# Kernel optimization log

Measured on AMD Instinct MI355X. Metric: run time of the kernel, lower is better.

Reference implementation:

```python
import jax, jax.numpy as jnp
import numpy as np

ALPHA = 0.25
GAMMA = 2.0
B, A, C, M = 8, 120000, 80, 32


def setup_inputs() -> dict:
    key = jax.random.key(0)
    k1, k2, k3, k4, k5, k6 = jax.random.split(key, 6)
    classifications = jax.random.uniform(k1, (B, A, C), jnp.float32)
    regressions = jax.random.normal(k2, (B, A, 4), jnp.float32)
    # anchors: valid x1<x2, y1<y2 boxes in a 1024x1024 image
    cx = jax.random.uniform(k3, (A,), jnp.float32, 0.0, 1024.0)
    cy = jax.random.uniform(k4, (A,), jnp.float32, 0.0, 1024.0)
    w = jax.random.uniform(jax.random.fold_in(k3, 1), (A,), jnp.float32, 16.0, 256.0)
    h = jax.random.uniform(jax.random.fold_in(k4, 1), (A,), jnp.float32, 16.0, 256.0)
    anchors = jnp.stack([cx - 0.5 * w, cy - 0.5 * h, cx + 0.5 * w, cy + 0.5 * h], axis=1)[None]
    # annotations: [x1,y1,x2,y2,label], all valid (label in [0, C))
    gcx = jax.random.uniform(k5, (B, M), jnp.float32, 64.0, 960.0)
    gcy = jax.random.uniform(jax.random.fold_in(k5, 1), (B, M), jnp.float32, 64.0, 960.0)
    gw = jax.random.uniform(jax.random.fold_in(k5, 2), (B, M), jnp.float32, 16.0, 256.0)
    gh = jax.random.uniform(jax.random.fold_in(k5, 3), (B, M), jnp.float32, 16.0, 256.0)
    labels = jax.random.randint(k6, (B, M), 0, C).astype(jnp.float32)
    annotations = jnp.stack(
        [gcx - 0.5 * gw, gcy - 0.5 * gh, gcx + 0.5 * gw, gcy + 0.5 * gh, labels], axis=2)
    return dict(classifications=classifications, regressions=regressions,
                anchors=anchors, annotations=annotations)


def _calc_iou(a, b):
    # a: [A,4] anchors, b: [M,4] gt boxes -> [A,M]
    area = (b[:, 2] - b[:, 0]) * (b[:, 3] - b[:, 1])
    iw = jnp.minimum(a[:, 2, None], b[None, :, 2]) - jnp.maximum(a[:, 0, None], b[None, :, 0])
    ih = jnp.minimum(a[:, 3, None], b[None, :, 3]) - jnp.maximum(a[:, 1, None], b[None, :, 1])
    inter = jnp.clip(iw, 0.0) * jnp.clip(ih, 0.0)
    ua = ((a[:, 2] - a[:, 0]) * (a[:, 3] - a[:, 1]))[:, None] + area[None, :] - inter
    return inter / jnp.clip(ua, 1e-8)


def _per_image(cls, reg, annots, anchor):
    valid = annots[:, 4] != -1.0  # padded gt boxes (label == -1) are ignored
    num_valid = valid.sum()
    cls = jnp.clip(cls, 1e-4, 1.0 - 1e-4)
    iou = jnp.where(valid[None, :], _calc_iou(anchor, annots[:, :4]), -1.0)  # [A,M]
    iou_max = iou.max(axis=1)
    iou_argmax = iou.argmax(axis=1)
    positive = iou_max >= 0.5
    num_pos = positive.sum()
    assigned = annots[iou_argmax]  # [A,5]
    nclass = cls.shape[1]
    # targets: -1 ignore; 0 where IoU<0.4 or positive; one-hot 1 at gt class for positives
    targets = jnp.full(cls.shape, -1.0, cls.dtype)
    targets = jnp.where((iou_max < 0.4)[:, None], 0.0, targets)
    onehot = jax.nn.one_hot(assigned[:, 4].astype(jnp.int32), nclass, dtype=cls.dtype)
    targets = jnp.where(positive[:, None], onehot, targets)
    alpha_factor = jnp.where(targets == 1.0, ALPHA, 1.0 - ALPHA)
    focal_w = alpha_factor * jnp.where(targets == 1.0, 1.0 - cls, cls) ** GAMMA
    bce = -(targets * jnp.log(cls) + (1.0 - targets) * jnp.log(1.0 - cls))
    cls_loss_mat = jnp.where(targets != -1.0, focal_w * bce, 0.0)
    npos_f = num_pos.astype(cls.dtype)
    cls_loss = cls_loss_mat.sum() / jnp.maximum(npos_f, 1.0)
    aw = anchor[:, 2] - anchor[:, 0]
    ah = anchor[:, 3] - anchor[:, 1]
    acx = anchor[:, 0] + 0.5 * aw
    acy = anchor[:, 1] + 0.5 * ah
    gw = assigned[:, 2] - assigned[:, 0]
    gh = assigned[:, 3] - assigned[:, 1]
    gcx = assigned[:, 0] + 0.5 * gw
    gcy = assigned[:, 1] + 0.5 * gh
    gw = jnp.maximum(gw, 1.0)
    gh = jnp.maximum(gh, 1.0)
    t = jnp.stack([(gcx - acx) / aw, (gcy - acy) / ah,
                   jnp.log(gw / aw), jnp.log(gh / ah)], axis=1)
    t = t / jnp.array([[0.1, 0.1, 0.2, 0.2]], t.dtype)
    diff = jnp.abs(t - reg)
    rl = jnp.where(diff <= 1.0 / 9.0, 0.5 * 9.0 * diff * diff, diff - 0.5 / 9.0)
    rl = jnp.where(positive[:, None], rl, 0.0)
    reg_loss = rl.sum() / jnp.maximum(npos_f * 4.0, 1.0)  # mean over [num_pos,4]
    reg_loss = jnp.where(num_pos > 0, reg_loss, 0.0)
    has = num_valid > 0
    return jnp.where(has, cls_loss, 0.0), jnp.where(has, reg_loss, 0.0)


def reference(classifications, regressions, anchors, annotations):
    anchor = anchors[0]
    cls_l, reg_l = jax.vmap(lambda c, r, a: _per_image(c, r, a, anchor))(
        classifications, regressions, annotations)
    return cls_l.mean(keepdims=True), reg_l.mean(keepdims=True)
```

## Files before the change

kernel.cpp:

```cpp
#include <hip/hip_runtime.h>

constexpr int B_IMG = 8;
constexpr int A_N   = 120000;
constexpr int C_N   = 80;
constexpr int M_N   = 32;

constexpr float ALPHA = 0.25f;

constexpr int BLK  = 256;
constexpr int APB  = 256;
constexpr int NBLK = (A_N + APB - 1) / APB;
constexpr int F4PA = C_N / 4;
constexpr int U    = 5;
constexpr int F4_PER_IT = BLK * U;
constexpr int NIT  = (APB * F4PA) / F4_PER_IT;

typedef float f4v __attribute__((ext_vector_type(4)));

__device__ __forceinline__ float smooth_l1(float d) {
    d = fabsf(d);
    return (d <= (1.0f / 9.0f)) ? 4.5f * d * d : d - (0.5f / 9.0f);
}

__device__ __forceinline__ float loss_neg(float x) {
    float p = fminf(fmaxf(x, 1e-4f), 0.9999f);
    return (1.0f - ALPHA) * p * p * (-__logf(1.0f - p));
}

__device__ __forceinline__ float loss_neg4(f4v v) {
    return loss_neg(v[0]) + loss_neg(v[1]) + loss_neg(v[2]) + loss_neg(v[3]);
}

__device__ __forceinline__ float loss_pos(float x) {
    float p = fminf(fmaxf(x, 1e-4f), 0.9999f);
    float q = 1.0f - p;
    return ALPHA * q * q * (-__logf(p));
}

__global__ __launch_bounds__(BLK, 4) void fused_kernel(
    const float* __restrict__ cls,
    const float* __restrict__ regressions,
    const float* __restrict__ anchors,
    const float* __restrict__ annotations,
    float* __restrict__ clsPart,
    float* __restrict__ regPart,
    float* __restrict__ nposPart)
{
    const int b    = blockIdx.y;
    const int base = blockIdx.x * APB;
    const int nA   = min(APB, A_N - base);
    const int t    = threadIdx.x;
    const int wave = t >> 6;
    const int lane = t & 63;
    const int a    = base + t;
    const bool full = (nA == APB);
    const bool inA  = (t < nA);

    __shared__ float smask[APB];

    const float* __restrict__ rowbase = cls + (size_t)(b * A_N + base) * C_N;
    const f4v* __restrict__ src = (const f4v*)rowbase;
    const f4v* __restrict__ pw = src + wave * (64 * U) + lane;
    const int widx0 = wave * (64 * U) + lane;

    float4 anc = make_float4(0.f, 0.f, 0.f, 0.f);
    if (inA) anc = ((const float4*)anchors)[a];

    f4v vA[U], vB[U];
    if (full) {
        #pragma unroll
        for (int u = 0; u < U; ++u) vA[u] = pw[u * 64];
        #pragma unroll
        for (int u = 0; u < U; ++u) vB[u] = pw[F4_PER_IT + u * 64];
    }

    const float* __restrict__ ann = annotations + (size_t)b * M_N * 5;
    int  bm = -1;
    bool positive = false, ignored = false;
    if (inA) {
        const float ax1 = anc.x, ay1 = anc.y, ax2 = anc.z, ay2 = anc.w;
        const float areaA = (ax2 - ax1) * (ay2 - ay1);
        float bi = -1.0f, bu = 1.0f;
        #pragma unroll 2
        for (int m = 0; m < M_N; ++m) {
            const float gx1 = ann[m * 5 + 0];
            const float gy1 = ann[m * 5 + 1];
            const float gx2 = ann[m * 5 + 2];
            const float gy2 = ann[m * 5 + 3];
            const bool valid = (ann[m * 5 + 4] != -1.0f);
            float iw = fminf(ax2, gx2) - fmaxf(ax1, gx1);
            float ih = fminf(ay2, gy2) - fmaxf(ay1, gy1);
            iw = fmaxf(iw, 0.0f);
            ih = fmaxf(ih, 0.0f);
            const float inter = iw * ih;
            const float areaB = (gx2 - gx1) * (gy2 - gy1);
            const float ua = fmaxf(areaA + areaB - inter, 1e-8f);
            const bool better = valid && (inter * bu > bi * ua);
            if (better) { bi = inter; bu = ua; bm = m; }
        }
        const float iouMax = (bm >= 0) ? (bi / bu) : -1.0f;
        positive = (iouMax >= 0.5f);
        ignored  = (iouMax >= 0.4f) && !positive;
    }
    smask[t] = (inA && !ignored) ? 1.0f : 0.0f;

    float regl = 0.0f, csum = 0.0f;
    const float pos = positive ? 1.0f : 0.0f;
    if (positive) {
        const float ax1 = anc.x, ay1 = anc.y, ax2 = anc.z, ay2 = anc.w;
        const float aw  = ax2 - ax1;
        const float ah  = ay2 - ay1;
        const float acx = ax1 + 0.5f * aw;
        const float acy = ay1 + 0.5f * ah;
        const float gx1 = ann[bm * 5 + 0];
        const float gy1 = ann[bm * 5 + 1];
        const float gx2 = ann[bm * 5 + 2];
        const float gy2 = ann[bm * 5 + 3];
        float gw = gx2 - gx1;
        float gh = gy2 - gy1;
        const float gcx = gx1 + 0.5f * gw;
        const float gcy = gy1 + 0.5f * gh;
        gw = fmaxf(gw, 1.0f);
        gh = fmaxf(gh, 1.0f);
        const float t0 = ((gcx - acx) / aw) * 10.0f;
        const float t1 = ((gcy - acy) / ah) * 10.0f;
        const float t2 = __logf(gw / aw) * 5.0f;
        const float t3 = __logf(gh / ah) * 5.0f;
        const float4 rg = ((const float4*)regressions)[(size_t)b * A_N + a];
        regl = smooth_l1(t0 - rg.x) + smooth_l1(t1 - rg.y) +
               smooth_l1(t2 - rg.z) + smooth_l1(t3 - rg.w);

        const int code = (int)ann[bm * 5 + 4];
        const float x = rowbase[(size_t)t * C_N + code];
        csum += loss_pos(x) - loss_neg(x);
    }
    __syncthreads();

    if (full) {
        #pragma unroll 1
        for (int it2 = 0; it2 < NIT / 2; ++it2) {
            const int it = it2 * 2;
            float pa = 0.0f;
            #pragma unroll
            for (int u = 0; u < U; ++u) {
                const unsigned idx = (unsigned)(it * F4_PER_IT + widx0 + u * 64);
                pa += smask[idx / 20u] * loss_neg4(vA[u]);
            }
            if (it + 2 < NIT) {
                #pragma unroll
                for (int u = 0; u < U; ++u)
                    vA[u] = pw[(it + 2) * F4_PER_IT + u * 64];
            }
            csum += pa;
            float pb = 0.0f;
            #pragma unroll
            for (int u = 0; u < U; ++u) {
                const unsigned idx = (unsigned)((it + 1) * F4_PER_IT + widx0 + u * 64);
                pb += smask[idx / 20u] * loss_neg4(vB[u]);
            }
            if (it + 3 < NIT) {
                #pragma unroll
                for (int u = 0; u < U; ++u)
                    vB[u] = pw[(it + 3) * F4_PER_IT + u * 64];
            }
            csum += pb;
        }
    } else {
        const int nF4 = nA * F4PA;
        for (int idx = t; idx < nF4; idx += BLK)
            csum += smask[(unsigned)idx / 20u] * loss_neg4(src[idx]);
    }

    float r = regl, p = pos, c = csum;
    #pragma unroll
    for (int off = 32; off; off >>= 1) {
        r += __shfl_down(r, off);
        p += __shfl_down(p, off);
        c += __shfl_down(c, off);
    }
    __shared__ float wr[BLK / 64], wp[BLK / 64], wc[BLK / 64];
    if (lane == 0) { wr[wave] = r; wp[wave] = p; wc[wave] = c; }
    __syncthreads();
    if (t == 0) {
        float rr = 0.0f, pp = 0.0f, cc = 0.0f;
        #pragma unroll
        for (int w = 0; w < BLK / 64; ++w) { rr += wr[w]; pp += wp[w]; cc += wc[w]; }
        const int pidx = b * NBLK + blockIdx.x;
        clsPart[pidx]  = cc;
        regPart[pidx]  = rr;
        nposPart[pidx] = pp;
    }
}

__global__ __launch_bounds__(64 * B_IMG) void finalize_kernel(
    const float* __restrict__ annotations,
    const float* __restrict__ clsPart,
    const float* __restrict__ regPart,
    const float* __restrict__ nposPart,
    float* __restrict__ out)
{
    const int w    = threadIdx.x >> 6;
    const int lane = threadIdx.x & 63;

    float c = 0.0f, r = 0.0f, p = 0.0f;
    for (int i = lane; i < NBLK; i += 64) {
        const int idx = w * NBLK + i;
        c += clsPart[idx];
        r += regPart[idx];
        p += nposPart[idx];
    }
    #pragma unroll
    for (int off = 32; off; off >>= 1) {
        c += __shfl_down(c, off);
        r += __shfl_down(r, off);
        p += __shfl_down(p, off);
    }

    __shared__ float sc[B_IMG], sr[B_IMG];
    if (lane == 0) {
        bool has = false;
        for (int m = 0; m < M_N; ++m)
            has = has || (annotations[(size_t)w * M_N * 5 + m * 5 + 4] != -1.0f);
        const float cl = c / fmaxf(p, 1.0f);
        const float rl = (p > 0.0f) ? r / (p * 4.0f) : 0.0f;
        sc[w] = has ? cl : 0.0f;
        sr[w] = has ? rl : 0.0f;
    }
    __syncthreads();
    if (threadIdx.x == 0) {
        float ca = 0.0f, ra = 0.0f;
        #pragma unroll
        for (int i = 0; i < B_IMG; ++i) { ca += sc[i]; ra += sr[i]; }
        out[0] = ca * (1.0f / B_IMG);
        out[1] = ra * (1.0f / B_IMG);
    }
}

extern "C" void kernel_launch(void* const* d_in, const int* in_sizes, int n_in,
                              void* d_out, int out_size, void* d_ws, size_t ws_size,
                              hipStream_t stream) {
    const float* classifications = (const float*)d_in[0];
    const float* regressions     = (const float*)d_in[1];
    const float* anchors         = (const float*)d_in[2];
    const float* annotations     = (const float*)d_in[3];
    float* out = (float*)d_out;

    float* clsPart  = (float*)d_ws;
    float* regPart  = clsPart + (size_t)B_IMG * NBLK;
    float* nposPart = regPart + (size_t)B_IMG * NBLK;

    fused_kernel<<<dim3(NBLK, B_IMG), BLK, 0, stream>>>(
        classifications, regressions, anchors, annotations,
        clsPart, regPart, nposPart);

    finalize_kernel<<<1, 64 * B_IMG, 0, stream>>>(
        annotations, clsPart, regPart, nposPart, out);
}
```

Measured before the change: 79.62 us.

## Fuse finalize into main kernel via last-block atomic, double anchors per block

The separate finalize kernel is removed: each workgroup writes its partials, fences, and bumps a global counter, and the last workgroup performs the final reduction. Each block now covers 512 anchors (two per thread for the IoU step) with a smaller unroll factor, which halves the grid and the number of partials. This targets the second kernel launch and its gap, but adds a memset before each call and an atomic per block. The larger per-block work also lowers the number of workgroups available for latency hiding.

```diff
diff --git a/kernel.cpp b/kernel.cpp
--- a/kernel.cpp
+++ b/kernel.cpp
@@ -8,10 +8,11 @@
 constexpr float ALPHA = 0.25f;
 
 constexpr int BLK  = 256;
-constexpr int APB  = 256;
+constexpr int APB  = 512;
 constexpr int NBLK = (A_N + APB - 1) / APB;
+constexpr int NWG  = NBLK * B_IMG;
 constexpr int F4PA = C_N / 4;
-constexpr int U    = 5;
+constexpr int U    = 4;
 constexpr int F4_PER_IT = BLK * U;
 constexpr int NIT  = (APB * F4PA) / F4_PER_IT;
 
@@ -35,6 +36,37 @@
     float p = fminf(fmaxf(x, 1e-4f), 0.9999f);
     float q = 1.0f - p;
     return ALPHA * q * q * (-__logf(p));
+}
+
+__device__ __forceinline__ void iou_one(
+    const float4 anc, const float* __restrict__ ann,
+    int& bm, bool& positive, bool& ignored)
+{
+    const float ax1 = anc.x, ay1 = anc.y, ax2 = anc.z, ay2 = anc.w;
+    const float areaA = (ax2 - ax1) * (ay2 - ay1);
+
+    float bi = -1.0f, bu = 1.0f;
+    bm = -1;
+    #pragma unroll 2
+    for (int m = 0; m < M_N; ++m) {
+        const float gx1 = ann[m * 5 + 0];
+        const float gy1 = ann[m * 5 + 1];
+        const float gx2 = ann[m * 5 + 2];
+        const float gy2 = ann[m * 5 + 3];
+        const bool valid = (ann[m * 5 + 4] != -1.0f);
+        float iw = fminf(ax2, gx2) - fmaxf(ax1, gx1);
+        float ih = fminf(ay2, gy2) - fmaxf(ay1, gy1);
+        iw = fmaxf(iw, 0.0f);
+        ih = fmaxf(ih, 0.0f);
+        const float inter = iw * ih;
+        const float areaB = (gx2 - gx1) * (gy2 - gy1);
+        const float ua = fmaxf(areaA + areaB - inter, 1e-8f);
+        const bool better = valid && (inter * bu > bi * ua);
+        if (better) { bi = inter; bu = ua; bm = m; }
+    }
+    const float iouMax = (bm >= 0) ? (bi / bu) : -1.0f;
+    positive = (iouMax >= 0.5f);
+    ignored  = (iouMax >= 0.4f) && !positive;
 }
 
 __global__ __launch_bounds__(BLK, 4) void fused_kernel(
@@ -42,29 +74,34 @@
     const float* __restrict__ regressions,
     const float* __restrict__ anchors,
     const float* __restrict__ annotations,
+    int*   __restrict__ counter,
     float* __restrict__ clsPart,
     float* __restrict__ regPart,
-    float* __restrict__ nposPart)
+    float* __restrict__ nposPart,
+    float* __restrict__ out)
 {
     const int b    = blockIdx.y;
     const int base = blockIdx.x * APB;
     const int nA   = min(APB, A_N - base);
+    const float* __restrict__ ann = annotations + (size_t)b * M_N * 5;
+
+    __shared__ float smask[APB];
+
     const int t    = threadIdx.x;
     const int wave = t >> 6;
     const int lane = t & 63;
-    const int a    = base + t;
     const bool full = (nA == APB);
-    const bool inA  = (t < nA);
-
-    __shared__ float smask[APB];
 
     const float* __restrict__ rowbase = cls + (size_t)(b * A_N + base) * C_N;
     const f4v* __restrict__ src = (const f4v*)rowbase;
     const f4v* __restrict__ pw = src + wave * (64 * U) + lane;
     const int widx0 = wave * (64 * U) + lane;
 
-    float4 anc = make_float4(0.f, 0.f, 0.f, 0.f);
-    if (inA) anc = ((const float4*)anchors)[a];
+    const bool v0 = (t < nA), v1 = (BLK + t < nA);
+    float4 anc0 = make_float4(0.f, 0.f, 0.f, 0.f);
+    float4 anc1 = anc0;
+    if (v0) anc0 = ((const float4*)anchors)[base + t];
+    if (v1) anc1 = ((const float4*)anchors)[base + BLK + t];
 
     f4v vA[U], vB[U];
     if (full) {
@@ -74,39 +111,24 @@
         for (int u = 0; u < U; ++u) vB[u] = pw[F4_PER_IT + u * 64];
     }
 
-    const float* __restrict__ ann = annotations + (size_t)b * M_N * 5;
-    int  bm = -1;
-    bool positive = false, ignored = false;
-    if (inA) {
-        const float ax1 = anc.x, ay1 = anc.y, ax2 = anc.z, ay2 = anc.w;
-        const float areaA = (ax2 - ax1) * (ay2 - ay1);
-        float bi = -1.0f, bu = 1.0f;
-        #pragma unroll 2
-        for (int m = 0; m < M_N; ++m) {
-            const float gx1 = ann[m * 5 + 0];
-            const float gy1 = ann[m * 5 + 1];
-            const float gx2 = ann[m * 5 + 2];
-            const float gy2 = ann[m * 5 + 3];
-            const bool valid = (ann[m * 5 + 4] != -1.0f);
-            float iw = fminf(ax2, gx2) - fmaxf(ax1, gx1);
-            float ih = fminf(ay2, gy2) - fmaxf(ay1, gy1);
-            iw = fmaxf(iw, 0.0f);
-            ih = fmaxf(ih, 0.0f);
-            const float inter = iw * ih;
-            const float areaB = (gx2 - gx1) * (gy2 - gy1);
-            const float ua = fmaxf(areaA + areaB - inter, 1e-8f);
-            const bool better = valid && (inter * bu > bi * ua);
-            if (better) { bi = inter; bu = ua; bm = m; }
-        }
-        const float iouMax = (bm >= 0) ? (bi / bu) : -1.0f;
-        positive = (iouMax >= 0.5f);
-        ignored  = (iouMax >= 0.4f) && !positive;
-    }
-    smask[t] = (inA && !ignored) ? 1.0f : 0.0f;
+    int  bm0, bm1;
+    bool pos0 = false, pos1 = false, ign0 = false, ign1 = false;
+    if (v0) iou_one(anc0, ann, bm0, pos0, ign0);
+    if (v1) iou_one(anc1, ann, bm1, pos1, ign1);
+    smask[t]       = (v0 && !ign0) ? 1.0f : 0.0f;
+    smask[BLK + t] = (v1 && !ign1) ? 1.0f : 0.0f;
+    __syncthreads();
 
     float regl = 0.0f, csum = 0.0f;
-    const float pos = positive ? 1.0f : 0.0f;
-    if (positive) {
+    float pcntf = (pos0 ? 1.0f : 0.0f) + (pos1 ? 1.0f : 0.0f);
+    #pragma unroll
+    for (int k = 0; k < 2; ++k) {
+        const bool  pos = k ? pos1 : pos0;
+        if (!pos) continue;
+        const int   bm  = k ? bm1  : bm0;
+        const float4 anc = k ? anc1 : anc0;
+        const int   li  = k * BLK + t;
+        const int   a   = base + li;
         const float ax1 = anc.x, ay1 = anc.y, ax2 = anc.z, ay2 = anc.w;
         const float aw  = ax2 - ax1;
         const float ah  = ay2 - ay1;
@@ -127,14 +149,13 @@
         const float t2 = __logf(gw / aw) * 5.0f;
         const float t3 = __logf(gh / ah) * 5.0f;
         const float4 rg = ((const float4*)regressions)[(size_t)b * A_N + a];
-        regl = smooth_l1(t0 - rg.x) + smooth_l1(t1 - rg.y) +
-               smooth_l1(t2 - rg.z) + smooth_l1(t3 - rg.w);
+        regl += smooth_l1(t0 - rg.x) + smooth_l1(t1 - rg.y) +
+                smooth_l1(t2 - rg.z) + smooth_l1(t3 - rg.w);
 
         const int code = (int)ann[bm * 5 + 4];
-        const float x = rowbase[(size_t)t * C_N + code];
+        const float x = rowbase[(size_t)li * C_N + code];
         csum += loss_pos(x) - loss_neg(x);
     }
-    __syncthreads();
 
     if (full) {
         #pragma unroll 1
@@ -167,11 +188,13 @@
         }
     } else {
         const int nF4 = nA * F4PA;
-        for (int idx = t; idx < nF4; idx += BLK)
-            csum += smask[(unsigned)idx / 20u] * loss_neg4(src[idx]);
-    }
-
-    float r = regl, p = pos, c = csum;
+        for (int idx = t; idx < nF4; idx += BLK) {
+            const f4v v = src[idx];
+            csum += smask[(unsigned)idx / 20u] * loss_neg4(v);
+        }
+    }
+
+    float r = regl, p = pcntf, c = csum;
     #pragma unroll
     for (int off = 32; off; off >>= 1) {
         r += __shfl_down(r, off);
@@ -181,6 +204,7 @@
     __shared__ float wr[BLK / 64], wp[BLK / 64], wc[BLK / 64];
     if (lane == 0) { wr[wave] = r; wp[wave] = p; wc[wave] = c; }
     __syncthreads();
+    __shared__ int isLast;
     if (t == 0) {
         float rr = 0.0f, pp = 0.0f, cc = 0.0f;
         #pragma unroll
@@ -189,50 +213,47 @@
         clsPart[pidx]  = cc;
         regPart[pidx]  = rr;
         nposPart[pidx] = pp;
-    }
-}
-
-__global__ __launch_bounds__(64 * B_IMG) void finalize_kernel(
-    const float* __restrict__ annotations,
-    const float* __restrict__ clsPart,
-    const float* __restrict__ regPart,
-    const float* __restrict__ nposPart,
-    float* __restrict__ out)
-{
-    const int w    = threadIdx.x >> 6;
-    const int lane = threadIdx.x & 63;
-
-    float c = 0.0f, r = 0.0f, p = 0.0f;
-    for (int i = lane; i < NBLK; i += 64) {
-        const int idx = w * NBLK + i;
-        c += clsPart[idx];
-        r += regPart[idx];
-        p += nposPart[idx];
-    }
-    #pragma unroll
-    for (int off = 32; off; off >>= 1) {
-        c += __shfl_down(c, off);
-        r += __shfl_down(r, off);
-        p += __shfl_down(p, off);
-    }
-
-    __shared__ float sc[B_IMG], sr[B_IMG];
-    if (lane == 0) {
-        bool has = false;
-        for (int m = 0; m < M_N; ++m)
-            has = has || (annotations[(size_t)w * M_N * 5 + m * 5 + 4] != -1.0f);
-        const float cl = c / fmaxf(p, 1.0f);
-        const float rl = (p > 0.0f) ? r / (p * 4.0f) : 0.0f;
-        sc[w] = has ? cl : 0.0f;
-        sr[w] = has ? rl : 0.0f;
+        __threadfence();
+        const int old = atomicAdd(counter, 1);
+        isLast = (old == NWG - 1) ? 1 : 0;
     }
     __syncthreads();
-    if (threadIdx.x == 0) {
-        float ca = 0.0f, ra = 0.0f;
-        #pragma unroll
-        for (int i = 0; i < B_IMG; ++i) { ca += sc[i]; ra += sr[i]; }
-        out[0] = ca * (1.0f / B_IMG);
-        out[1] = ra * (1.0f / B_IMG);
+
+    if (isLast) {
+        __threadfence();
+        __shared__ float sc[B_IMG], sr[B_IMG];
+        for (int w = wave; w < B_IMG; w += BLK / 64) {
+            float fc = 0.0f, fr = 0.0f, fp = 0.0f;
+            for (int i = lane; i < NBLK; i += 64) {
+                const int idx = w * NBLK + i;
+                fc += clsPart[idx];
+                fr += regPart[idx];
+                fp += nposPart[idx];
+            }
+            #pragma unroll
+            for (int off = 32; off; off >>= 1) {
+                fc += __shfl_down(fc, off);
+                fr += __shfl_down(fr, off);
+                fp += __shfl_down(fp, off);
+            }
+            if (lane == 0) {
+                bool has = false;
+                for (int m = 0; m < M_N; ++m)
+                    has = has || (annotations[(size_t)w * M_N * 5 + m * 5 + 4] != -1.0f);
+                const float cl = fc / fmaxf(fp, 1.0f);
+                const float rl = (fp > 0.0f) ? fr / (fp * 4.0f) : 0.0f;
+                sc[w] = has ? cl : 0.0f;
+                sr[w] = has ? rl : 0.0f;
+            }
+        }
+        __syncthreads();
+        if (t == 0) {
+            float ca = 0.0f, ra = 0.0f;
+            #pragma unroll
+            for (int i = 0; i < B_IMG; ++i) { ca += sc[i]; ra += sr[i]; }
+            out[0] = ca * (1.0f / B_IMG);
+            out[1] = ra * (1.0f / B_IMG);
+        }
     }
 }
 
@@ -245,14 +266,14 @@
     const float* annotations     = (const float*)d_in[3];
     float* out = (float*)d_out;
 
-    float* clsPart  = (float*)d_ws;
+    int*   counter  = (int*)d_ws;
+    float* clsPart  = (float*)((char*)d_ws + 16);
     float* regPart  = clsPart + (size_t)B_IMG * NBLK;
     float* nposPart = regPart + (size_t)B_IMG * NBLK;
 
+    hipMemsetAsync(counter, 0, 16, stream);
+
     fused_kernel<<<dim3(NBLK, B_IMG), BLK, 0, stream>>>(
         classifications, regressions, anchors, annotations,
-        clsPart, regPart, nposPart);
-
-    finalize_kernel<<<1, 64 * B_IMG, 0, stream>>>(
-        annotations, clsPart, regPart, nposPart, out);
-}
+        counter, clsPart, regPart, nposPart, out);
+}
```

Result: slower. 161.0 us (+102.2%).
